# Kernel optimization log

Hardware: AMD Instinct MI355X
Metric: run time of the kernel (lower is better)

The kernel has to match this reference:

```python
import jax, jax.numpy as jnp
import numpy as np

INPUT_SIZE = 608
STRIDE = 32
NUM_CLASSES = 20
NMS_THRESH = 0.5
NUM_ANCHOR = 5
ANCHORS = np.array([[1.19, 1.98], [2.79, 4.59], [4.53, 8.92], [8.06, 5.29], [10.32, 10.65]], dtype=np.float32)


def _conv(x, w, b, pad):
    # x: NCHW, w: OIHW
    y = jax.lax.conv_general_dilated(x, w, (1, 1), [(pad, pad), (pad, pad)],
                                     dimension_numbers=('NCHW', 'OIHW', 'NCHW'))
    return y + b[None, :, None, None]


def _leaky(x):
    return jnp.where(x > 0, x, 0.1 * x)


def _reorg(x, s=2):
    # space-to-depth, darknet reorg: [B,C,H,W] -> [B,C*s*s,H/s,W/s]
    B, C, H, W = x.shape
    x = x.reshape(B, C, H // s, s, W // s, s)
    x = x.transpose(0, 3, 5, 1, 2, 4)
    return x.reshape(B, C * s * s, H // s, W // s)


def _forward_boxes_scores(feat_layer2, feat_layer3, w1a, b1a, w1b, b1b, wr, br, w2, b2, wp, bp):
    p5 = _leaky(_conv(feat_layer3, w1a, b1a, 1))
    p5 = _leaky(_conv(p5, w1b, b1b, 1))
    p4 = _reorg(_leaky(_conv(feat_layer2, wr, br, 0)))         # [1,256,19,19]
    p5 = jnp.concatenate([p4, p5], axis=1)                      # [1,1280,19,19]
    p5 = _leaky(_conv(p5, w2, b2, 1))
    pred = _conv(p5, wp, bp, 0)                                 # [1,125,19,19]
    B, C, H, W = pred.shape
    pred = pred.transpose(0, 2, 3, 1).reshape(B, H * W, C)
    conf = pred[:, :, :NUM_ANCHOR].reshape(B, H * W * NUM_ANCHOR, 1)
    cls = pred[:, :, NUM_ANCHOR:(1 + NUM_CLASSES) * NUM_ANCHOR].reshape(B, H * W * NUM_ANCHOR, NUM_CLASSES)
    reg = pred[:, :, (1 + NUM_CLASSES) * NUM_ANCHOR:].reshape(B, H * W, NUM_ANCHOR, 4)
    # decode_xywh
    gy, gx = jnp.meshgrid(jnp.arange(H), jnp.arange(W), indexing='ij')
    grid = jnp.stack([gx, gy], axis=-1).astype(pred.dtype).reshape(1, H * W, 1, 2)
    anchor_wh = jnp.asarray(ANCHORS).reshape(1, 1, NUM_ANCHOR, 2)
    xy = jax.nn.sigmoid(reg[..., :2]) + grid
    wh = jnp.exp(reg[..., 2:]) * anchor_wh
    xywh = jnp.concatenate([xy, wh], axis=-1).reshape(B, -1, 4) * STRIDE
    boxes = jnp.concatenate([xywh[..., :2] - 0.5 * xywh[..., 2:],
                             xywh[..., :2] + 0.5 * xywh[..., 2:]], axis=-1)
    boxes = jnp.clip(boxes[0] / INPUT_SIZE, 0.0, 1.0)           # [N,4]
    scores = jax.nn.sigmoid(conf[0]) * jax.nn.softmax(cls[0], axis=-1)  # [N,20]
    return boxes, scores


def _per_class_nms(boxes, scores, class_mask):
    # greedy sequential NMS, faithful to the torch while-loop (suppress iff IoU > thresh)
    N = boxes.shape[0]
    s = jnp.where(class_mask, scores, -jnp.inf)
    order = jnp.argsort(-s)
    b = boxes[order]
    valid = class_mask[order]
    x1, y1, x2, y2 = b[:, 0], b[:, 1], b[:, 2], b[:, 3]
    areas = (x2 - x1) * (y2 - y1)
    iw = jnp.maximum(1e-10, jnp.minimum(x2[:, None], x2[None, :]) - jnp.maximum(x1[:, None], x1[None, :]))
    ih = jnp.maximum(1e-10, jnp.minimum(y2[:, None], y2[None, :]) - jnp.maximum(y1[:, None], y1[None, :]))
    inter = iw * ih
    iou = inter / (areas[:, None] + areas[None, :] - inter)
    upper = jnp.arange(N)[None, :] > jnp.arange(N)[:, None]
    sup_mat = (iou > NMS_THRESH) & upper

    def body(i, state):
        suppressed, keep = state
        cur = valid[i] & jnp.logical_not(suppressed[i])
        keep = keep.at[i].set(cur)
        suppressed = suppressed | (cur & sup_mat[i])
        return suppressed, keep

    _, keep_sorted = jax.lax.fori_loop(0, N, body, (jnp.zeros(N, bool), jnp.zeros(N, bool)))
    return jnp.zeros(N, bool).at[order].set(keep_sorted)


def setup_inputs() -> dict:
    key = jax.random.key(0)
    ks = jax.random.split(key, 8)
    w = lambda k, shape: jax.random.normal(k, shape, jnp.float32) * 0.01
    return {
        'feat_layer2': jax.random.normal(ks[0], (1, 512, 38, 38), jnp.float32),
        'feat_layer3': jax.random.normal(ks[1], (1, 1024, 19, 19), jnp.float32),
        'w1a': w(ks[2], (1024, 1024, 3, 3)), 'b1a': jnp.zeros((1024,), jnp.float32),
        'w1b': w(ks[3], (1024, 1024, 3, 3)), 'b1b': jnp.zeros((1024,), jnp.float32),
        'wr': w(ks[4], (64, 512, 1, 1)), 'br': jnp.zeros((64,), jnp.float32),
        'w2': w(ks[5], (1024, 1280, 3, 3)), 'b2': jnp.zeros((1024,), jnp.float32),
        'wp': w(ks[6], (125, 1024, 1, 1)), 'bp': jnp.zeros((125,), jnp.float32),
    }


def reference(feat_layer2, feat_layer3, w1a, b1a, w1b, b1b, wr, br, w2, b2, wp, bp):
    boxes, scores_full = _forward_boxes_scores(feat_layer2, feat_layer3,
                                               w1a, b1a, w1b, b1b, wr, br, w2, b2, wp, bp)
    cls_inds = jnp.argmax(scores_full, axis=1)                          # [N]
    scores = jnp.take_along_axis(scores_full, cls_inds[:, None], axis=1)[:, 0]
    masks = cls_inds[None, :] == jnp.arange(NUM_CLASSES)[:, None]       # [20,N]
    keeps = jax.vmap(lambda m: _per_class_nms(boxes, scores, m))(masks)
    keep = jnp.any(keeps, axis=0)                                       # [N] bool, fixed-shape mask
    return boxes, scores, cls_inds, keep
```

## Files before the change

### kernel.cpp

```cpp
#include <hip/hip_runtime.h>

typedef _Float16 f16;
typedef _Float16 f16x8 __attribute__((ext_vector_type(8)));
typedef float f32x4 __attribute__((ext_vector_type(4)));

#define N_BOX 1805
#define NPIX 361
#define NCLS 20
#define MCAP 320
#define GNW 29

__device__ __forceinline__ float leakyf(float x){ return x > 0.f ? x : 0.1f*x; }
__device__ __forceinline__ float sigmoidf_(float x){ return 1.f/(1.f + expf(-x)); }

__global__ void transpose_k(const float* __restrict__ src, float* __restrict__ dst, int R, int C){
  int i = blockIdx.x*256 + threadIdx.x;
  if (i < R*C){ int r = i / C, c = i % C; dst[c*R + r] = src[i]; }
}

__global__ void wprep_k(const float* __restrict__ w, f16* __restrict__ whi, f16* __restrict__ wlo,
                        int Cin, int total){
  int i = blockIdx.x*256 + threadIdx.x;
  if (i >= total) return;
  int co = i / Cin, ci = i - co*Cin;
  const float* src = w + (size_t)i*9;
  int K9 = 9*Cin;
  size_t dbase = (size_t)co*K9 + ci;
  #pragma unroll
  for (int t = 0; t < 9; ++t){
    float v = src[t]*64.f;
    f16 hi = (f16)v;
    f16 lo = (f16)(v - (float)hi);
    whi[dbase + (size_t)t*Cin] = hi;
    wlo[dbase + (size_t)t*Cin] = lo;
  }
}

__global__ void act1prep_k(const float* __restrict__ feat3, f16* __restrict__ ah, f16* __restrict__ al){
  int i = blockIdx.x*256 + threadIdx.x;
  if (i >= NPIX*1024) return;
  int p = i >> 10, c = i & 1023;
  float v = feat3[c*NPIX + p];
  f16 hi = (f16)v; f16 lo = (f16)(v - (float)hi);
  ah[i] = hi; al[i] = lo;
}

__global__ __launch_bounds__(256) void reorg_conv_k(const float* __restrict__ feat2,
    const float* __restrict__ wrT, const float* __restrict__ br,
    f16* __restrict__ cath, f16* __restrict__ catl){
  int c  = threadIdx.x & 63;
  int pq = threadIdx.x >> 6;
  int pix = blockIdx.x*4 + pq;
  int y = pix / 38, x = pix % 38;
  __shared__ float s_in[64][4];
  float acc = br[c];
  for (int cb = 0; cb < 512; cb += 64){
    __syncthreads();
    { int k = threadIdx.x >> 2, pp = threadIdx.x & 3;
      s_in[k][pp] = feat2[(cb + k)*1444 + blockIdx.x*4 + pp]; }
    __syncthreads();
    #pragma unroll
    for (int k = 0; k < 64; ++k)
      acc = fmaf(wrT[(cb+k)*64 + c], s_in[k][pq], acc);
  }
  float v = leakyf(acc);
  int co = ((y & 1)*2 + (x & 1))*64 + c;
  int p = (y>>1)*19 + (x>>1);
  f16 hi = (f16)v; f16 lo = (f16)(v - (float)hi);
  size_t o = (size_t)p*1280 + co;
  cath[o] = hi; catl[o] = lo;
}

__global__ __launch_bounds__(256) void conv_mfma_k(
    const f16* __restrict__ whi, const f16* __restrict__ wlo,
    const f16* __restrict__ ahi, const f16* __restrict__ alo,
    float* __restrict__ part, int Cin, int chunks, int cpt)
{
  const int K9 = 9*Cin;
  int cob = blockIdx.x * 128;
  int px0 = blockIdx.y * 128;
  int ks  = blockIdx.z;
  int kc0 = ks * chunks;
  int tid = threadIdx.x;

  __shared__ f16 sAh[128*32], sAl[128*32], sBh[128*32], sBl[128*32];

  int r = tid >> 1, h = tid & 1;
  int wb0 = ((r*64 + h*32)      ) ^ ((r&7)<<4);
  int wb1 = ((r*64 + h*32 + 16) ) ^ ((r&7)<<4);
  const f16* wArowh = whi + (size_t)(cob + r)*K9 + h*16;
  const f16* wArowl = wlo + (size_t)(cob + r)*K9 + h*16;
  int p = px0 + r;
  int py = p / 19, px = p - py*19;

  int lane = tid & 63, wid = tid >> 6;
  int lrow = lane & 15, lgrp = lane >> 4;
  int wr = wid >> 1, wc = wid & 1;
  int swz = (lrow & 7) << 4;
  int aoff[4], boff[4];
  #pragma unroll
  for (int m = 0; m < 4; ++m){
    int rA = wr*64 + m*16 + lrow;
    aoff[m] = (rA*64 + lgrp*16) ^ swz;
    int rB = wc*64 + m*16 + lrow;
    boff[m] = (rB*64 + lgrp*16) ^ swz;
  }

  f32x4 acc[4][4] = {};

  for (int kc = kc0; kc < kc0 + chunks; ++kc){
    int t = kc / cpt;
    int ci0 = (kc - t*cpt) * 32;
    int dy = t / 3, dx = t - dy*3;
    int yy = py + dy - 1, xx = px + dx - 1;
    bool bvalid = (p < NPIX) && ((unsigned)yy < 19u) && ((unsigned)xx < 19u);

    f16x8 a0 = *(const f16x8*)(wArowh + (size_t)kc*32);
    f16x8 a1 = *(const f16x8*)(wArowh + (size_t)kc*32 + 8);
    f16x8 a2 = *(const f16x8*)(wArowl + (size_t)kc*32);
    f16x8 a3 = *(const f16x8*)(wArowl + (size_t)kc*32 + 8);
    f16x8 b0 = {}, b1 = {}, b2 = {}, b3 = {};
    if (bvalid){
      const f16* bh_src = ahi + (size_t)(yy*19+xx)*Cin + ci0 + h*16;
      const f16* bl_src = alo + (size_t)(yy*19+xx)*Cin + ci0 + h*16;
      b0 = *(const f16x8*)(bh_src);
      b1 = *(const f16x8*)(bh_src + 8);
      b2 = *(const f16x8*)(bl_src);
      b3 = *(const f16x8*)(bl_src + 8);
    }
    __syncthreads();
    *(f16x8*)((char*)sAh + wb0) = a0; *(f16x8*)((char*)sAh + wb1) = a1;
    *(f16x8*)((char*)sAl + wb0) = a2; *(f16x8*)((char*)sAl + wb1) = a3;
    *(f16x8*)((char*)sBh + wb0) = b0; *(f16x8*)((char*)sBh + wb1) = b1;
    *(f16x8*)((char*)sBl + wb0) = b2; *(f16x8*)((char*)sBl + wb1) = b3;
    __syncthreads();

    f16x8 bh[4], bl[4];
    #pragma unroll
    for (int n = 0; n < 4; ++n){
      bh[n] = *(const f16x8*)((char*)sBh + boff[n]);
      bl[n] = *(const f16x8*)((char*)sBl + boff[n]);
    }
    #pragma unroll
    for (int m = 0; m < 4; ++m){
      f16x8 ah = *(const f16x8*)((char*)sAh + aoff[m]);
      f16x8 al = *(const f16x8*)((char*)sAl + aoff[m]);
      #pragma unroll
      for (int n = 0; n < 4; ++n){
        acc[m][n] = __builtin_amdgcn_mfma_f32_16x16x32_f16(ah, bh[n], acc[m][n], 0,0,0);
        acc[m][n] = __builtin_amdgcn_mfma_f32_16x16x32_f16(ah, bl[n], acc[m][n], 0,0,0);
        acc[m][n] = __builtin_amdgcn_mfma_f32_16x16x32_f16(al, bh[n], acc[m][n], 0,0,0);
      }
    }
  }

  #pragma unroll
  for (int m = 0; m < 4; ++m){
    #pragma unroll
    for (int n = 0; n < 4; ++n){
      int pp = px0 + wc*64 + n*16 + lrow;
      if (pp < NPIX){
        int co = cob + wr*64 + m*16 + lgrp*4;
        size_t base = ((size_t)ks*1024 + co)*NPIX + pp;
        part[base          ] = acc[m][n][0];
        part[base +   NPIX ] = acc[m][n][1];
        part[base + 2*NPIX ] = acc[m][n][2];
        part[base + 3*NPIX ] = acc[m][n][3];
      }
    }
  }
}

__global__ void reduce16v_k(const float* __restrict__ part, const float* __restrict__ bias,
                            f16* __restrict__ dhi, f16* __restrict__ dlo,
                            int Cstride, int Coff, int splitk){
  int i = blockIdx.x*256 + threadIdx.x;
  if (i >= 1024*NPIX) return;
  int co = i / NPIX, p = i - co*NPIX;
  float s = 0.f;
  for (int k = 0; k < splitk; ++k) s += part[(size_t)k*1024*NPIX + i];
  float v = leakyf(s*0.015625f + bias[co]);
  f16 hi = (f16)v;
  f16 lo = (f16)(v - (float)hi);
  size_t o = (size_t)p*Cstride + Coff + co;
  dhi[o] = hi; dlo[o] = lo;
}

__global__ __launch_bounds__(256) void pred_conv_k(const f16* __restrict__ a3h, const f16* __restrict__ a3l,
    const float* __restrict__ wpT, const float* __restrict__ bp, float* __restrict__ pred){
  int c = threadIdx.x & 127, ph = threadIdx.x >> 7;
  int pix = blockIdx.x*2 + ph;
  __shared__ float s_in[64][2];
  float acc = 0.f;
  for (int cb = 0; cb < 1024; cb += 64){
    __syncthreads();
    if (threadIdx.x < 128){
      int k = threadIdx.x & 63, pp = threadIdx.x >> 6;
      int px2 = blockIdx.x*2 + pp;
      float v = 0.f;
      if (px2 < NPIX){
        size_t o = (size_t)px2*1024 + cb + k;
        v = (float)a3h[o] + (float)a3l[o];
      }
      s_in[k][pp] = v;
    }
    __syncthreads();
    if (c < 125){
      #pragma unroll
      for (int k = 0; k < 64; ++k)
        acc = fmaf(wpT[(cb+k)*125 + c], s_in[k][ph], acc);
    }
  }
  if (c < 125 && pix < NPIX) pred[c*NPIX + pix] = acc + bp[c];
}

__device__ const float ANCW[5] = {1.19f, 2.79f, 4.53f, 8.06f, 10.32f};
__device__ const float ANCH_[5] = {1.98f, 4.59f, 8.92f, 5.29f, 10.65f};

__global__ void decode_k(const float* __restrict__ pred, float* __restrict__ out,
                         int* __restrict__ cls_i, int* __restrict__ cnt){
  int n = blockIdx.x*256 + threadIdx.x;
  if (blockIdx.x == 0 && threadIdx.x < NCLS) cnt[threadIdx.x] = 0;
  if (n >= N_BOX) return;
  int p = n / 5, a = n % 5;
  float conf = pred[a*NPIX + p];
  float cl[20]; float m = -1e30f;
  #pragma unroll
  for (int k = 0; k < 20; ++k){ cl[k] = pred[(5 + a*20 + k)*NPIX + p]; m = fmaxf(m, cl[k]); }
  float s = 0.f;
  #pragma unroll
  for (int k = 0; k < 20; ++k){ cl[k] = expf(cl[k]-m); s += cl[k]; }
  int bi = 0; float bv = cl[0];
  #pragma unroll
  for (int k = 1; k < 20; ++k) if (cl[k] > bv){ bv = cl[k]; bi = k; }
  float score = sigmoidf_(conf) * (bv / s);
  float tx = pred[(105 + a*4 + 0)*NPIX + p];
  float ty = pred[(105 + a*4 + 1)*NPIX + p];
  float tw = pred[(105 + a*4 + 2)*NPIX + p];
  float th = pred[(105 + a*4 + 3)*NPIX + p];
  float gx = (float)(p % 19), gy = (float)(p / 19);
  float cx = (sigmoidf_(tx) + gx) * 32.f;
  float cy = (sigmoidf_(ty) + gy) * 32.f;
  float bw = expf(tw) * ANCW[a] * 32.f;
  float bh = expf(th) * ANCH_[a] * 32.f;
  float x1 = fminf(fmaxf((cx - 0.5f*bw) / 608.f, 0.f), 1.f);
  float y1 = fminf(fmaxf((cy - 0.5f*bh) / 608.f, 0.f), 1.f);
  float x2 = fminf(fmaxf((cx + 0.5f*bw) / 608.f, 0.f), 1.f);
  float y2 = fminf(fmaxf((cy + 0.5f*bh) / 608.f, 0.f), 1.f);
  out[n*4+0]=x1; out[n*4+1]=y1; out[n*4+2]=x2; out[n*4+3]=y2;
  out[7220 + n]  = score;
  out[9025 + n]  = (float)bi;
  out[10830 + n] = 0.f;
  cls_i[n] = bi;
}

__global__ __launch_bounds__(256) void rank_k(const float* __restrict__ scores,
    const int* __restrict__ cls_i, int* __restrict__ ord, int* __restrict__ cnt){
  __shared__ float s_sc[N_BOX];
  __shared__ short s_cl[N_BOX];
  int tid = threadIdx.x;
  for (int j = tid; j < N_BOX; j += 256){ s_sc[j] = scores[j]; s_cl[j] = (short)cls_i[j]; }
  __syncthreads();
  int wid = tid >> 6, lane = tid & 63;
  int i = blockIdx.x*4 + wid;
  if (i >= N_BOX) return;
  float si = s_sc[i]; short ci = s_cl[i];
  int r = 0;
  for (int j = lane; j < N_BOX; j += 64){
    float sj = s_sc[j];
    r += (int)((s_cl[j] == ci) & ((sj > si) | ((sj == si) & (j < i))));
  }
  #pragma unroll
  for (int o = 32; o; o >>= 1) r += __shfl_down(r, o);
  if (lane == 0){
    ord[ci*N_BOX + r] = i;
    atomicAdd(&cnt[ci], 1);
  }
}

__global__ __launch_bounds__(256) void nms2_k(const float* __restrict__ boxes,
    const int* __restrict__ ord, const int* __restrict__ cnt, float* __restrict__ keep,
    unsigned long long* __restrict__ gmask){
  __shared__ float X1[N_BOX], Y1[N_BOX], X2[N_BOX], Y2[N_BOX], AR[N_BOX];
  __shared__ int IDX[N_BOX];
  __shared__ unsigned long long smask[MCAP*(MCAP/64 + 1)];
  int c = blockIdx.x, tid = threadIdx.x;
  int n = cnt[c];
  if (n <= 0) return;
  for (int t = tid; t < n; t += 256){
    int bi = ord[c*N_BOX + t];
    float x1 = boxes[bi*4+0], y1 = boxes[bi*4+1], x2 = boxes[bi*4+2], y2 = boxes[bi*4+3];
    X1[t]=x1; Y1[t]=y1; X2[t]=x2; Y2[t]=y2; AR[t]=(x2-x1)*(y2-y1);
    IDX[t]=bi;
  }
  __syncthreads();
  int nw = (n + 63) >> 6;
  bool lds = (n <= MCAP);
  unsigned long long* rows = lds ? smask : (gmask + (size_t)c*N_BOX*GNW);
  for (int task = tid; task < n*nw; task += 256){
    int i = task / nw, w = task - i*nw;
    float ax1=X1[i], ay1=Y1[i], ax2=X2[i], ay2=Y2[i], areaA=AR[i];
    unsigned long long bits = 0;
    int j0 = w << 6;
    int jb = i+1 > j0 ? i+1 : j0;
    int je = j0+64 < n ? j0+64 : n;
    for (int j = jb; j < je; ++j){
      float iw = fmaxf(1e-10f, fminf(ax2,X2[j]) - fmaxf(ax1,X1[j]));
      float ih = fmaxf(1e-10f, fminf(ay2,Y2[j]) - fmaxf(ay1,Y1[j]));
      float inter = iw*ih;
      float iou = inter / (areaA + AR[j] - inter);
      bits |= (unsigned long long)(iou > 0.5f) << (j - j0);
    }
    rows[(size_t)i*nw + w] = bits;
  }
  __syncthreads();
  if (tid < 64){
    int lane = tid;
    unsigned long long S = 0;
    unsigned long long r0,r1,r2,r3;
    bool act = lane < nw;
    r0 = (act && 0 < n) ? rows[lane] : 0ull;
    r1 = (act && 1 < n) ? rows[(size_t)1*nw + lane] : 0ull;
    r2 = (act && 2 < n) ? rows[(size_t)2*nw + lane] : 0ull;
    r3 = (act && 3 < n) ? rows[(size_t)3*nw + lane] : 0ull;
    for (int i = 0; i < n; ++i){
      unsigned long long row = r0; r0 = r1; r1 = r2; r2 = r3;
      r3 = (act && i+4 < n) ? rows[(size_t)(i+4)*nw + lane] : 0ull;
      unsigned long long Siw = __shfl(S, i >> 6);
      if (!((Siw >> (i & 63)) & 1ull)){
        if (lane == 0) keep[IDX[i]] = 1.f;
        S |= row;
      }
    }
  }
}

static inline size_t align256(size_t x){ return (x + 255) & ~(size_t)255; }

extern "C" void kernel_launch(void* const* d_in, const int* in_sizes, int n_in,
                              void* d_out, int out_size, void* d_ws, size_t ws_size,
                              hipStream_t stream){
  const float* feat2 = (const float*)d_in[0];
  const float* feat3 = (const float*)d_in[1];
  const float* w1a = (const float*)d_in[2];
  const float* b1a = (const float*)d_in[3];
  const float* w1b = (const float*)d_in[4];
  const float* b1b = (const float*)d_in[5];
  const float* wr  = (const float*)d_in[6];
  const float* br  = (const float*)d_in[7];
  const float* w2  = (const float*)d_in[8];
  const float* b2  = (const float*)d_in[9];
  const float* wp  = (const float*)d_in[10];
  const float* bp  = (const float*)d_in[11];
  float* out = (float*)d_out;
  char* ws = (char*)d_ws;

  size_t off = 0;
  float* part = (float*)(ws + off); off = align256(off + (size_t)16*1024*NPIX*4);
  f16* wh   = (f16*)(ws + off); off = align256(off + (size_t)1024*1280*9*2);
  f16* wl   = (f16*)(ws + off); off = align256(off + (size_t)1024*1280*9*2);
  f16* a1h  = (f16*)(ws + off); off = align256(off + (size_t)NPIX*1024*2);
  f16* a1l  = (f16*)(ws + off); off = align256(off + (size_t)NPIX*1024*2);
  f16* a2h  = (f16*)(ws + off); off = align256(off + (size_t)NPIX*1024*2);
  f16* a2l  = (f16*)(ws + off); off = align256(off + (size_t)NPIX*1024*2);
  f16* a3h  = (f16*)(ws + off); off = align256(off + (size_t)NPIX*1024*2);
  f16* a3l  = (f16*)(ws + off); off = align256(off + (size_t)NPIX*1024*2);
  f16* cath = (f16*)(ws + off); off = align256(off + (size_t)NPIX*1280*2);
  f16* catl = (f16*)(ws + off); off = align256(off + (size_t)NPIX*1280*2);
  float* pred = (float*)(ws + off); off = align256(off + (size_t)125*NPIX*4);
  float* wrT  = (float*)(ws + off); off = align256(off + (size_t)512*64*4);
  float* wpT  = (float*)(ws + off); off = align256(off + (size_t)1024*125*4);
  int* cls_i  = (int*)(ws + off); off = align256(off + (size_t)N_BOX*4);
  int* ord    = (int*)(ws + off); off = align256(off + (size_t)NCLS*N_BOX*4);
  int* cnt    = (int*)(ws + off); off = align256(off + (size_t)NCLS*4);
  unsigned long long* gmask = (unsigned long long*)part;

  transpose_k<<<(64*512 + 255)/256, 256, 0, stream>>>(wr, wrT, 64, 512);
  transpose_k<<<(125*1024 + 255)/256, 256, 0, stream>>>(wp, wpT, 125, 1024);
  act1prep_k<<<(NPIX*1024 + 255)/256, 256, 0, stream>>>(feat3, a1h, a1l);
  reorg_conv_k<<<361, 256, 0, stream>>>(feat2, wrT, br, cath, catl);

  wprep_k<<<(1024*1024 + 255)/256, 256, 0, stream>>>(w1a, wh, wl, 1024, 1024*1024);
  { dim3 g(8, 3, 16);
    conv_mfma_k<<<g, 256, 0, stream>>>(wh, wl, a1h, a1l, part, 1024, 18, 32); }
  reduce16v_k<<<(1024*NPIX + 255)/256, 256, 0, stream>>>(part, b1a, a2h, a2l, 1024, 0, 16);

  wprep_k<<<(1024*1024 + 255)/256, 256, 0, stream>>>(w1b, wh, wl, 1024, 1024*1024);
  { dim3 g(8, 3, 16);
    conv_mfma_k<<<g, 256, 0, stream>>>(wh, wl, a2h, a2l, part, 1024, 18, 32); }
  reduce16v_k<<<(1024*NPIX + 255)/256, 256, 0, stream>>>(part, b1b, cath, catl, 1280, 256, 16);

  wprep_k<<<(1024*1280 + 255)/256, 256, 0, stream>>>(w2, wh, wl, 1280, 1024*1280);
  { dim3 g(8, 3, 15);
    conv_mfma_k<<<g, 256, 0, stream>>>(wh, wl, cath, catl, part, 1280, 24, 40); }
  reduce16v_k<<<(1024*NPIX + 255)/256, 256, 0, stream>>>(part, b2, a3h, a3l, 1024, 0, 15);

  pred_conv_k<<<181, 256, 0, stream>>>(a3h, a3l, wpT, bp, pred);
  decode_k<<<8, 256, 0, stream>>>(pred, out, cls_i, cnt);
  rank_k<<<(N_BOX + 3)/4, 256, 0, stream>>>(out + 7220, cls_i, ord, cnt);
  nms2_k<<<NCLS, 256, 0, stream>>>(out, ord, cnt, out + 10830, gmask);
}
```

Before: 340.6 us.

## Split NMS into parallel chunked mask build and word-serial greedy scan

The per-class NMS kernel is split in two. A mask-building kernel is launched over class × 8 row-chunks so the IoU bitmask is computed by many more blocks, and it always writes to a global mask with a fixed row stride. A separate one-wave scan kernel then walks the mask 64 boxes at a time, resolving keeps within each word through the diagonal block using readlane and ctz, instead of looping serially over every box. This trades the LDS mask fast path for small classes and an extra launch for more parallelism in the mask build and a shorter serial scan.

```diff
diff --git a/kernel.cpp b/kernel.cpp
--- a/kernel.cpp
+++ b/kernel.cpp
@@ -7,8 +7,8 @@
 #define N_BOX 1805
 #define NPIX 361
 #define NCLS 20
-#define MCAP 320
 #define GNW 29
+#define MB_ROWS 226
 
 __device__ __forceinline__ float leakyf(float x){ return x > 0.f ? x : 0.1f*x; }
 __device__ __forceinline__ float sigmoidf_(float x){ return 1.f/(1.f + expf(-x)); }
@@ -278,27 +278,27 @@
   }
 }
 
-__global__ __launch_bounds__(256) void nms2_k(const float* __restrict__ boxes,
-    const int* __restrict__ ord, const int* __restrict__ cnt, float* __restrict__ keep,
+__global__ __launch_bounds__(256) void maskbuild_k(const float* __restrict__ boxes,
+    const int* __restrict__ ord, const int* __restrict__ cnt,
     unsigned long long* __restrict__ gmask){
   __shared__ float X1[N_BOX], Y1[N_BOX], X2[N_BOX], Y2[N_BOX], AR[N_BOX];
-  __shared__ int IDX[N_BOX];
-  __shared__ unsigned long long smask[MCAP*(MCAP/64 + 1)];
-  int c = blockIdx.x, tid = threadIdx.x;
+  int c = blockIdx.x, chunk = blockIdx.y, tid = threadIdx.x;
   int n = cnt[c];
-  if (n <= 0) return;
+  int r0 = chunk*MB_ROWS;
+  if (n <= 0 || r0 >= n) return;
+  int r1 = r0 + MB_ROWS; if (r1 > n) r1 = n;
+  int rows_here = r1 - r0;
   for (int t = tid; t < n; t += 256){
     int bi = ord[c*N_BOX + t];
     float x1 = boxes[bi*4+0], y1 = boxes[bi*4+1], x2 = boxes[bi*4+2], y2 = boxes[bi*4+3];
     X1[t]=x1; Y1[t]=y1; X2[t]=x2; Y2[t]=y2; AR[t]=(x2-x1)*(y2-y1);
-    IDX[t]=bi;
   }
   __syncthreads();
   int nw = (n + 63) >> 6;
-  bool lds = (n <= MCAP);
-  unsigned long long* rows = lds ? smask : (gmask + (size_t)c*N_BOX*GNW);
-  for (int task = tid; task < n*nw; task += 256){
-    int i = task / nw, w = task - i*nw;
+  unsigned long long* rows = gmask + (size_t)c*N_BOX*GNW;
+  for (int task = tid; task < rows_here*nw; task += 256){
+    int w = task / rows_here, ri = task - w*rows_here;
+    int i = r0 + ri;
     float ax1=X1[i], ay1=Y1[i], ax2=X2[i], ay2=Y2[i], areaA=AR[i];
     unsigned long long bits = 0;
     int j0 = w << 6;
@@ -311,27 +311,52 @@
       float iou = inter / (areaA + AR[j] - inter);
       bits |= (unsigned long long)(iou > 0.5f) << (j - j0);
     }
-    rows[(size_t)i*nw + w] = bits;
-  }
+    rows[(size_t)i*GNW + w] = bits;
+  }
+}
+
+__global__ __launch_bounds__(64) void nmsscan_k(const int* __restrict__ ord,
+    const int* __restrict__ cnt, const unsigned long long* __restrict__ gmask,
+    float* __restrict__ keep){
+  __shared__ int sidx[N_BOX];
+  int c = blockIdx.x, lane = threadIdx.x;
+  int n = cnt[c];
+  if (n <= 0) return;
+  int nw = (n + 63) >> 6;
+  for (int t = lane; t < n; t += 64) sidx[t] = ord[c*N_BOX + t];
   __syncthreads();
-  if (tid < 64){
-    int lane = tid;
-    unsigned long long S = 0;
-    unsigned long long r0,r1,r2,r3;
-    bool act = lane < nw;
-    r0 = (act && 0 < n) ? rows[lane] : 0ull;
-    r1 = (act && 1 < n) ? rows[(size_t)1*nw + lane] : 0ull;
-    r2 = (act && 2 < n) ? rows[(size_t)2*nw + lane] : 0ull;
-    r3 = (act && 3 < n) ? rows[(size_t)3*nw + lane] : 0ull;
-    for (int i = 0; i < n; ++i){
-      unsigned long long row = r0; r0 = r1; r1 = r2; r2 = r3;
-      r3 = (act && i+4 < n) ? rows[(size_t)(i+4)*nw + lane] : 0ull;
-      unsigned long long Siw = __shfl(S, i >> 6);
-      if (!((Siw >> (i & 63)) & 1ull)){
-        if (lane == 0) keep[IDX[i]] = 1.f;
-        S |= row;
-      }
-    }
+  const unsigned long long* rows = gmask + (size_t)c*N_BOX*GNW;
+  bool act = lane < nw;
+  unsigned long long S = 0;
+  unsigned long long diag = (lane < n) ? rows[(size_t)lane*GNW + 0] : 0ull;
+  for (int w = 0; w < nw; ++w){
+    int base = w << 6;
+    int nb = n - base; if (nb > 64) nb = 64;
+    unsigned int slo = (unsigned)__builtin_amdgcn_readlane((int)(unsigned)S, w);
+    unsigned int shi = (unsigned)__builtin_amdgcn_readlane((int)(unsigned)(S >> 32), w);
+    unsigned long long sup = ((unsigned long long)shi << 32) | slo;
+    unsigned long long validm = (nb >= 64) ? ~0ull : ((1ull << nb) - 1ull);
+    unsigned long long avail = ~sup & validm;
+    unsigned long long kmask = 0;
+    unsigned long long diag_next = 0;
+    if (w+1 < nw){
+      int i2 = base + 64 + lane;
+      if (i2 < n) diag_next = rows[(size_t)i2*GNW + (w+1)];
+    }
+    while (avail){
+      int b = __builtin_ctzll(avail);
+      kmask |= 1ull << b;
+      unsigned int dlo = (unsigned)__builtin_amdgcn_readlane((int)(unsigned)diag, b);
+      unsigned int dhi = (unsigned)__builtin_amdgcn_readlane((int)(unsigned)(diag >> 32), b);
+      unsigned long long drow = ((unsigned long long)dhi << 32) | dlo;
+      sup |= drow;
+      avail &= ~(1ull << b);
+      avail &= ~sup;
+      if (act && lane > w)
+        S |= rows[(size_t)(base + b)*GNW + lane];
+    }
+    if ((kmask >> lane) & 1ull) keep[sidx[base + lane]] = 1.f;
+    diag = diag_next;
   }
 }
 
@@ -398,5 +423,7 @@
   pred_conv_k<<<181, 256, 0, stream>>>(a3h, a3l, wpT, bp, pred);
   decode_k<<<8, 256, 0, stream>>>(pred, out, cls_i, cnt);
   rank_k<<<(N_BOX + 3)/4, 256, 0, stream>>>(out + 7220, cls_i, ord, cnt);
-  nms2_k<<<NCLS, 256, 0, stream>>>(out, ord, cnt, out + 10830, gmask);
-}
+  { dim3 mg(NCLS, 8);
+    maskbuild_k<<<mg, 256, 0, stream>>>(out, ord, cnt, gmask); }
+  nmsscan_k<<<NCLS, 64, 0, stream>>>(ord, cnt, gmask, out + 10830);
+}
```

New measurement: 318.2 us. 1.07x faster.
